# Kernel optimization log

Measured on AMD Instinct MI355X. Metric: run time of the kernel, lower is better.

The kernel has to match this reference:

```python
import jax, jax.numpy as jnp
import numpy as np

B, T, E, H = 4, 2048, 2048, 16
HD = E // H  # 128


def apply_rope(x, freqs):
    # x: (B, T, H, HD); freqs: (T, HD//2) rotation angles per position/pair
    cos = jnp.cos(freqs)[None, :, None, :]  # (1, T, 1, HD//2)
    sin = jnp.sin(freqs)[None, :, None, :]
    xr = x.reshape(*x.shape[:-1], HD // 2, 2)
    x1, x2 = xr[..., 0], xr[..., 1]
    out = jnp.stack([x1 * cos - x2 * sin, x1 * sin + x2 * cos], axis=-1)
    return out.reshape(x.shape)


def setup_inputs() -> dict:
    key = jax.random.key(0)
    k1, k2, k3, k4 = jax.random.split(key, 4)
    x = jax.random.normal(k1, (B, T, E), dtype=jnp.float32)
    freqs = jax.random.uniform(k2, (T, HD // 2), dtype=jnp.float32) * 6.28318
    w_qkv = jax.random.normal(k3, (3 * E, E), dtype=jnp.float32) * 0.02
    w_o = jax.random.normal(k4, (E, E), dtype=jnp.float32) * 0.02
    return {"x": x, "freqs": freqs, "w_qkv": w_qkv, "w_o": w_o}


def reference(x, freqs, w_qkv, w_o):
    b, t, e = x.shape
    qkv = x @ w_qkv.T                            # (B, T, 3E)
    qkv = qkv.reshape(b, t, 3, H, HD)
    q, k, v = qkv[:, :, 0], qkv[:, :, 1], qkv[:, :, 2]
    q = apply_rope(q, freqs)
    k = apply_rope(k, freqs)
    q = q.transpose(0, 2, 1, 3)                  # (B, H, T, HD)
    k = k.transpose(0, 2, 1, 3)
    v = v.transpose(0, 2, 1, 3)
    scale = 1.0 / np.sqrt(HD)
    scores = jnp.einsum('bhqd,bhkd->bhqk', q, k) * scale
    causal = jnp.tril(jnp.ones((t, t), dtype=bool))
    scores = jnp.where(causal[None, None], scores, jnp.finfo(scores.dtype).min)
    attn = jax.nn.softmax(scores, axis=-1)
    out = jnp.einsum('bhqk,bhkd->bhqd', attn, v)  # (B, H, T, HD)
    out = out.transpose(0, 2, 1, 3).reshape(b, t, e)
    return out @ w_o.T
```

## Files before the change

### kernel.cpp

```cpp
#include <hip/hip_runtime.h>
#include <type_traits>

#define DEV __device__ __forceinline__

typedef __attribute__((ext_vector_type(4))) float f32x4;
typedef __attribute__((ext_vector_type(8))) __bf16 bf16x8;
typedef __attribute__((ext_vector_type(8))) short s16x8;
typedef unsigned int u32;
typedef unsigned short u16;

DEV u16 f2bf(float f) {
  u32 u = __builtin_bit_cast(u32, f);
  u32 r = u + 0x7FFFu + ((u >> 16) & 1u);
  return (u16)(r >> 16);
}
DEV float bf2f(u16 h) {
  u32 u = ((u32)h) << 16;
  return __builtin_bit_cast(float, u);
}

template <typename A>
DEV auto mfma_sel(A a, A b, f32x4 c, int)
    -> decltype(__builtin_amdgcn_mfma_f32_16x16x32_bf16(a, b, c, 0, 0, 0)) {
  return __builtin_amdgcn_mfma_f32_16x16x32_bf16(a, b, c, 0, 0, 0);
}
template <typename A>
DEV f32x4 mfma_sel(A a, A b, f32x4 c, long) {
  using O = typename std::conditional<std::is_same<A, bf16x8>::value, s16x8, bf16x8>::type;
  return __builtin_amdgcn_mfma_f32_16x16x32_bf16(
      __builtin_bit_cast(O, a), __builtin_bit_cast(O, b), c, 0, 0, 0);
}
DEV f32x4 MFMA16(bf16x8 a, bf16x8 b, f32x4 c) { return mfma_sel(a, b, c, 0); }

DEV void gload_lds16(const void* g, void* l) {
  __builtin_amdgcn_global_load_lds(
      (__attribute__((address_space(1))) void*)(g),
      (__attribute__((address_space(3))) void*)(l), 16, 0, 0);
}

__global__ __launch_bounds__(256) void cvt_f32_bf16(const float* __restrict__ in,
                                                    u16* __restrict__ out, int n4) {
  int i = blockIdx.x * blockDim.x + threadIdx.x;
  const int stride = gridDim.x * blockDim.x;
  for (; i < n4; i += stride) {
    const float4 v = ((const float4*)in)[i];
    ushort4 o;
    o.x = f2bf(v.x); o.y = f2bf(v.y); o.z = f2bf(v.z); o.w = f2bf(v.w);
    ((ushort4*)out)[i] = o;
  }
}

__global__ __launch_bounds__(256) void build_tab(const float* __restrict__ freqs,
                                                 float* __restrict__ ct,
                                                 float* __restrict__ st, int n) {
  int i = blockIdx.x * blockDim.x + threadIdx.x;
  if (i < n) {
    float f = freqs[i];
    ct[i] = cosf(f);
    st[i] = sinf(f);
  }
}

template <bool OBF>
__global__ __launch_bounds__(512, 2) void gemm_bt(const u16* __restrict__ A,
                                                  const u16* __restrict__ Bm,
                                                  void* __restrict__ Cp,
                                                  const int M, const int N, const int K) {
  __shared__ __align__(16) u16 As[4][256 * 32];
  __shared__ __align__(16) u16 Bs[4][256 * 32];
  const int tid = threadIdx.x;
  const int wid = tid >> 6;
  const int lane = tid & 63;
  const int lrow = lane & 15;
  const int lgrp = lane >> 4;

  const int gx = gridDim.x;
  const int nwg = gx * gridDim.y;
  int id = blockIdx.y * gx + blockIdx.x;
  const int cpx = nwg >> 3;
  id = (id & 7) * cpx + (id >> 3);
  const int row0 = (id / gx) * 256;
  const int col0 = (id % gx) * 256;

  const int wm = (wid >> 2) * 128;
  const int wn = (wid & 3) * 64;

  f32x4 acc[8][4] = {};

  const int sj0 = wid * 2;
  const int srow = lane >> 2;
  const int sc = lane & 3;

#define STAGE_HALF(SLOT, T, II)                                                   \
  do {                                                                            \
    const int j_ = sj0 + (II);                                                    \
    const int row_ = j_ * 16 + srow;                                              \
    const int ch_ = sc ^ ((row_ >> 1) & 3);                                       \
    const int k0_ = (T) * 32;                                                     \
    gload_lds16(A + (size_t)(row0 + row_) * K + k0_ + ch_ * 8,                    \
                (char*)&As[SLOT][0] + j_ * 1024);                                 \
    gload_lds16(Bm + (size_t)(col0 + row_) * K + k0_ + ch_ * 8,                   \
                (char*)&Bs[SLOT][0] + j_ * 1024);                                 \
  } while (0)

#define READS_B(SLOT)                                                             \
  _Pragma("unroll") for (int fn = 0; fn < 4; ++fn) {                              \
    const int brow_ = wn + fn * 16 + lrow;                                        \
    bfr[fn] = *(const bf16x8*)((const char*)&Bs[SLOT][0] + brow_ * 64 +           \
                               ((lgrp ^ ((brow_ >> 1) & 3)) << 4));               \
  }

#define READS_A(SLOT, QUAD)                                                       \
  _Pragma("unroll") for (int i_ = 0; i_ < 4; ++i_) {                              \
    const int arow_ = wm + ((QUAD) * 4 + i_) * 16 + lrow;                         \
    af[i_] = *(const bf16x8*)((const char*)&As[SLOT][0] + arow_ * 64 +            \
                              ((lgrp ^ ((arow_ >> 1) & 3)) << 4));                \
  }

#define MFMA_QUAD(QUAD)                                                           \
  __builtin_amdgcn_s_setprio(1);                                                  \
  _Pragma("unroll") for (int fm = 0; fm < 4; ++fm) {                              \
    _Pragma("unroll") for (int fn = 0; fn < 4; ++fn)                              \
      acc[(QUAD) * 4 + fm][fn] = MFMA16(af[fm], bfr[fn], acc[(QUAD) * 4 + fm][fn]); \
  }                                                                               \
  __builtin_amdgcn_s_setprio(0);

  const int nk = K >> 5;
  STAGE_HALF(0, 0, 0); STAGE_HALF(0, 0, 1);
  STAGE_HALF(1, 1, 0); STAGE_HALF(1, 1, 1);
  STAGE_HALF(2, 2, 0); STAGE_HALF(2, 2, 1);
  __builtin_amdgcn_sched_barrier(0);
  asm volatile("s_waitcnt vmcnt(8)" ::: "memory");
  __builtin_amdgcn_s_barrier();

  bf16x8 bfr[4], af[4];
  for (int t = 0; t < nk - 2; ++t) {
    const int slot = t & 3;
    const int ns = (t + 3) & 3;
    const bool dostage = (t + 3) < nk;
    READS_B(slot)
    READS_A(slot, 0)
    if (dostage) STAGE_HALF(ns, t + 3, 0);
    __builtin_amdgcn_sched_barrier(0);
    __builtin_amdgcn_s_barrier();
    MFMA_QUAD(0)
    __builtin_amdgcn_sched_barrier(0);
    __builtin_amdgcn_s_barrier();
    READS_A(slot, 1)
    if (dostage) STAGE_HALF(ns, t + 3, 1);
    __builtin_amdgcn_sched_barrier(0);
    __builtin_amdgcn_s_barrier();
    MFMA_QUAD(1)
    __builtin_amdgcn_sched_barrier(0);
    asm volatile("s_waitcnt vmcnt(8)" ::: "memory");
    __builtin_amdgcn_s_barrier();
  }
  {
    const int slot = (nk - 2) & 3;
    READS_B(slot) READS_A(slot, 0)
    __builtin_amdgcn_sched_barrier(0);
    __builtin_amdgcn_s_barrier();
    MFMA_QUAD(0)
    __builtin_amdgcn_s_barrier();
    READS_A(slot, 1)
    __builtin_amdgcn_sched_barrier(0);
    __builtin_amdgcn_s_barrier();
    MFMA_QUAD(1)
    __builtin_amdgcn_sched_barrier(0);
    asm volatile("s_waitcnt vmcnt(0)" ::: "memory");
    __builtin_amdgcn_s_barrier();
  }
  {
    const int slot = (nk - 1) & 3;
    READS_B(slot) READS_A(slot, 0)
    __builtin_amdgcn_sched_barrier(0);
    __builtin_amdgcn_s_barrier();
    MFMA_QUAD(0)
    __builtin_amdgcn_s_barrier();
    READS_A(slot, 1)
    MFMA_QUAD(1)
  }

  #pragma unroll
  for (int fm = 0; fm < 8; ++fm) {
    #pragma unroll
    for (int r = 0; r < 4; ++r) {
      const size_t rb = (size_t)(row0 + wm + fm * 16 + lgrp * 4 + r) * N + col0 + wn + lrow;
      #pragma unroll
      for (int fn = 0; fn < 4; ++fn) {
        if constexpr (OBF)
          ((u16*)Cp)[rb + fn * 16] = f2bf(acc[fm][fn][r]);
        else
          ((float*)Cp)[rb + fn * 16] = acc[fm][fn][r];
      }
    }
  }
#undef STAGE_HALF
#undef READS_B
#undef READS_A
#undef MFMA_QUAD
}

__global__ __launch_bounds__(256) void rope_rearrange(const u16* __restrict__ qkv,
                                                      const float* __restrict__ ct,
                                                      const float* __restrict__ st,
                                                      u16* __restrict__ q_r,
                                                      u16* __restrict__ k_r,
                                                      u16* __restrict__ vt) {
  constexpr int T = 2048;
  constexpr int H = 16;
  __shared__ u16 tile[64][130];
  const int tt = blockIdx.x, h = blockIdx.y, b = blockIdx.z;
  const int t0 = tt * 64;
  const int tid = threadIdx.x;
  const int r = t0 + (tid >> 2);
  const int cg = (tid & 3) * 32;
  const int bh = b * H + h;

  #pragma unroll
  for (int which = 0; which < 2; ++which) {
    const u16* src = qkv + ((((size_t)b * T + r) * 3 + which) * H + h) * 128 + cg;
    u16* dst = (which == 0 ? q_r : k_r) + ((size_t)bh * T + r) * 128 + cg;
    const u32* su = (const u32*)src;
    u32* du = (u32*)dst;
    const int pb = r * 64 + (cg >> 1);
    #pragma unroll
    for (int p = 0; p < 16; ++p) {
      const u32 v = su[p];
      const float x1 = bf2f((u16)(v & 0xffff));
      const float x2 = bf2f((u16)(v >> 16));
      const float c = ct[pb + p];
      const float sn = st[pb + p];
      const float o1 = x1 * c - x2 * sn;
      const float o2 = x1 * sn + x2 * c;
      du[p] = (u32)f2bf(o1) | ((u32)f2bf(o2) << 16);
    }
  }

  {
    const u16* src = qkv + ((((size_t)b * T + r) * 3 + 2) * H + h) * 128 + cg;
    const int tl = tid >> 2;
    #pragma unroll
    for (int jj = 0; jj < 32; ++jj)
      tile[tl][cg + jj] = src[jj];
  }
  __syncthreads();
  {
    const int d = tid >> 1, half = tid & 1;
    u16* dst = vt + ((size_t)bh * 128 + d) * T + t0 + half * 32;
    #pragma unroll
    for (int jj = 0; jj < 32; ++jj)
      dst[jj] = tile[half * 32 + jj][d];
  }
}

__global__ __launch_bounds__(512, 2) void attn_fwd(const u16* __restrict__ Qp,
                                                   const u16* __restrict__ Kp,
                                                   const u16* __restrict__ Vp,
                                                   u16* __restrict__ Op) {
  constexpr int T = 2048;
  __shared__ __align__(16) u16 Kl[3][64 * 128];
  __shared__ __align__(16) u16 Vl[3][128 * 64];
  __shared__ __align__(16) u16 Pl[8 * 1024];

  const int tid = threadIdx.x;
  const int wid = tid >> 6;
  const int lane = tid & 63;
  const int lrow = lane & 15;
  const int lgrp = lane >> 4;

  const int lin = blockIdx.y * 4 + blockIdx.x;
  const int qa = lin >> 6;
  const int bh = ((lin & 7) << 3) | ((lin >> 3) & 7);

  const u16* Qb = Qp + (size_t)bh * T * 128;
  const u16* Kb = Kp + (size_t)bh * T * 128;
  const u16* Vb = Vp + (size_t)bh * 128 * T;

  const float CE = 0.08838834765f * 1.44269504089f;
  const float DTH = 12.0f / CE;
  const int s0 = (lane & 48) + ((lane & 48) >> 2);
  char* Pw = (char*)Pl + wid * 2048;
  const int ob = bh >> 4, oh = bh & 15;

  auto stage = [&](int buf, int kv0) {
    #pragma unroll
    for (int ii = 0; ii < 2; ++ii) {
      const int i = wid * 2 + ii;
      {
        const int rr = i * 4 + (lane >> 4);
        const int cs = (lane & 15) ^ (rr & 7);
        gload_lds16(Kb + (size_t)(kv0 + rr) * 128 + cs * 8, (char*)&Kl[buf][0] + i * 1024);
      }
      {
        const int rr = i * 8 + (lane >> 3);
        const int cs = (lane & 7) ^ (rr & 7);
        gload_lds16(Vb + (size_t)rr * T + kv0 + cs * 8, (char*)&Vl[buf][0] + i * 1024);
      }
    }
  };

  auto process = [&](const int qi) {
    const int q0 = qi * 256;
    const int wq0 = q0 + wid * 32;

    bf16x8 qf[2][4];
    #pragma unroll
    for (int qg = 0; qg < 2; ++qg) {
      const int qrow = wq0 + qg * 16 + lrow;
      #pragma unroll
      for (int db = 0; db < 4; ++db)
        qf[qg][db] = *(const bf16x8*)(Qb + (size_t)qrow * 128 + db * 32 + lgrp * 8);
    }

    f32x4 o[2][8] = {};
    float m[2] = {-3e38f, -3e38f};
    float l[2] = {0.f, 0.f};

    const int nkv = 4 * qi + 4;
    stage(0, 0);
    stage(1, 64);
    int cs = 0;
    for (int j = 0; j < nkv; ++j) {
      __builtin_amdgcn_sched_barrier(0);
      if (j < nkv - 1) {
        asm volatile("s_waitcnt vmcnt(4)" ::: "memory");
      } else {
        asm volatile("s_waitcnt vmcnt(0)" ::: "memory");
      }
      __builtin_amdgcn_s_barrier();
      if (j + 2 < nkv) {
        int ss = cs + 2; if (ss >= 3) ss -= 3;
        stage(ss, (j + 2) * 64);
      }
      const int kv0 = j * 64;

      if (kv0 <= wq0 + 31) {
        f32x4 s[2][4] = {};
        #pragma unroll
        for (int t4 = 0; t4 < 4; ++t4) {
          const int krow = t4 * 16 + lrow;
          #pragma unroll
          for (int db = 0; db < 4; ++db) {
            const int ch = (db * 4 + lgrp) ^ (krow & 7);
            bf16x8 kf = *(const bf16x8*)((const char*)&Kl[cs][0] + krow * 256 + ch * 16);
            s[0][t4] = MFMA16(kf, qf[0][db], s[0][t4]);
            s[1][t4] = MFMA16(kf, qf[1][db], s[1][t4]);
          }
        }

        if (kv0 + 63 > wq0) {
          #pragma unroll
          for (int qg = 0; qg < 2; ++qg) {
            const int lim = wq0 + qg * 16 + lrow - kv0 - lgrp * 4;
            #pragma unroll
            for (int t4 = 0; t4 < 4; ++t4) {
              #pragma unroll
              for (int r = 0; r < 4; ++r)
                if (t4 * 16 + r > lim) s[qg][t4][r] = -3e38f;
            }
          }
        }

        float pmax[2];
        #pragma unroll
        for (int qg = 0; qg < 2; ++qg) {
          float pm = fmaxf(fmaxf(s[qg][0][0], s[qg][0][1]), fmaxf(s[qg][0][2], s[qg][0][3]));
          #pragma unroll
          for (int t4 = 1; t4 < 4; ++t4)
            pm = fmaxf(pm, fmaxf(fmaxf(s[qg][t4][0], s[qg][t4][1]),
                                 fmaxf(s[qg][t4][2], s[qg][t4][3])));
          pm = fmaxf(pm, __shfl_xor(pm, 16));
          pm = fmaxf(pm, __shfl_xor(pm, 32));
          pmax[qg] = pm;
        }

        float alpha[2] = {1.f, 1.f};
        const float dmax = fmaxf(pmax[0] - m[0], pmax[1] - m[1]);
        if (__any(dmax > DTH)) {
          #pragma unroll
          for (int qg = 0; qg < 2; ++qg) {
            const float mn = fmaxf(m[qg], pmax[qg]);
            alpha[qg] = exp2f((m[qg] - mn) * CE);
            m[qg] = mn;
          }
          #pragma unroll
          for (int qg = 0; qg < 2; ++qg) {
            #pragma unroll
            for (int r = 0; r < 4; ++r) {
              const float a4 = __shfl(alpha[qg], s0 + r);
              #pragma unroll
              for (int db = 0; db < 8; ++db)
                o[qg][db][r] *= a4;
            }
          }
        }

        #pragma unroll
        for (int qg = 0; qg < 2; ++qg) {
          float psum = 0.f;
          #pragma unroll
          for (int t4 = 0; t4 < 4; ++t4) {
            #pragma unroll
            for (int r = 0; r < 4; ++r) {
              const float p = exp2f((s[qg][t4][r] - m[qg]) * CE);
              s[qg][t4][r] = p;
              psum += p;
            }
          }
          psum += __shfl_xor(psum, 16);
          psum += __shfl_xor(psum, 32);
          l[qg] = l[qg] * alpha[qg] + psum;

          #pragma unroll
          for (int t4 = 0; t4 < 4; ++t4) {
            uint2 w;
            w.x = (u32)f2bf(s[qg][t4][0]) | ((u32)f2bf(s[qg][t4][1]) << 16);
            w.y = (u32)f2bf(s[qg][t4][2]) | ((u32)f2bf(s[qg][t4][3]) << 16);
            const int off = lrow * 128 + (((t4 * 2 + (lgrp >> 1)) ^ (lrow & 7)) << 4) + (lgrp & 1) * 8;
            *(uint2*)(Pw + off) = w;
          }
          asm volatile("s_waitcnt lgkmcnt(0)" ::: "memory");
          __builtin_amdgcn_sched_barrier(0);

          bf16x8 pa[2];
          #pragma unroll
          for (int kb = 0; kb < 2; ++kb)
            pa[kb] = *(const bf16x8*)(Pw + lrow * 128 + (((kb * 4 + lgrp) ^ (lrow & 7)) << 4));
          #pragma unroll
          for (int db = 0; db < 8; ++db) {
            const int vrow = db * 16 + lrow;
            #pragma unroll
            for (int kb = 0; kb < 2; ++kb) {
              const int vch = (kb * 4 + lgrp) ^ (vrow & 7);
              bf16x8 vf = *(const bf16x8*)((const char*)&Vl[cs][0] + vrow * 128 + vch * 16);
              o[qg][db] = MFMA16(pa[kb], vf, o[qg][db]);
            }
          }
        }
      }
      cs = (cs == 2) ? 0 : cs + 1;
    }

    #pragma unroll
    for (int qg = 0; qg < 2; ++qg) {
      const float inv = 1.f / l[qg];
      float inv4[4];
      #pragma unroll
      for (int r = 0; r < 4; ++r) inv4[r] = __shfl(inv, s0 + r);
      #pragma unroll
      for (int db = 0; db < 8; ++db) {
        #pragma unroll
        for (int r = 0; r < 4; ++r) {
          const int qrow = wq0 + qg * 16 + lgrp * 4 + r;
          Op[((size_t)ob * T + qrow) * 2048 + oh * 128 + db * 16 + lrow] =
              f2bf(o[qg][db][r] * inv4[r]);
        }
      }
    }
  };

  process(7 - qa);
  __syncthreads();
  process(qa);
}

extern "C" void kernel_launch(void* const* d_in, const int* in_sizes, int n_in,
                              void* d_out, int out_size, void* d_ws, size_t ws_size,
                              hipStream_t stream) {
  const float* x = (const float*)d_in[0];
  const float* freqs = (const float*)d_in[1];
  const float* w_qkv = (const float*)d_in[2];
  const float* w_o = (const float*)d_in[3];

  constexpr int B = 4, T = 2048, E = 2048, H = 16;
  constexpr size_t M = (size_t)B * T;
  constexpr int N3 = 3 * E;

  char* ws = (char*)d_ws;
  size_t off = 0;
  auto alloc = [&](size_t bytes) {
    void* p = ws + off;
    off += (bytes + 255) & ~(size_t)255;
    return p;
  };
  u16* wqkv_bf = (u16*)alloc((size_t)N3 * E * 2);
  u16* wo_bf   = (u16*)alloc((size_t)E * E * 2);
  u16* x_bf    = (u16*)alloc(M * E * 2);
  u16* qkv_bf  = (u16*)alloc(M * (size_t)N3 * 2);
  u16* k_r     = (u16*)alloc(M * E * 2);
  u16* vt      = (u16*)alloc(M * E * 2);
  float* ct    = (float*)alloc((size_t)T * 64 * 4);
  float* st    = (float*)alloc((size_t)T * 64 * 4);
  u16* q_r = x_bf;
  u16* attn_o = qkv_bf;

  cvt_f32_bf16<<<2048, 256, 0, stream>>>(x, x_bf, (int)(M * E / 4));
  cvt_f32_bf16<<<2048, 256, 0, stream>>>(w_qkv, wqkv_bf, N3 * E / 4);
  cvt_f32_bf16<<<2048, 256, 0, stream>>>(w_o, wo_bf, E * E / 4);
  build_tab<<<(T * 64) / 256, 256, 0, stream>>>(freqs, ct, st, T * 64);

  gemm_bt<true><<<dim3(N3 / 256, (int)(M / 256)), 512, 0, stream>>>(
      x_bf, wqkv_bf, qkv_bf, (int)M, N3, E);
  rope_rearrange<<<dim3(T / 64, H, B), 256, 0, stream>>>(qkv_bf, ct, st, q_r, k_r, vt);
  attn_fwd<<<dim3(4, B * H), 512, 0, stream>>>(q_r, k_r, vt, attn_o);
  gemm_bt<false><<<dim3(E / 256, (int)(M / 256)), 512, 0, stream>>>(
      attn_o, wo_bf, d_out, (int)M, E, E);
}
```

Before: 483.4 us.

## Deepen attention K/V prefetch to four stages and unify GEMM main loop

The attention kernel's K/V shared-memory ring grows from 3 to 4 slots, so three tiles are prefetched ahead instead of two. The vmcnt wait thresholds are adjusted for the deeper queue, and slot indexing becomes a simple j&3. The GEMM loop folds its two peeled tail iterations into the main loop, with vmcnt waits chosen per iteration. It also places the workgroup barrier before an explicit lgkmcnt(0) wait ahead of each MFMA quad. The deeper ring raises LDS use to about 144KB per block, which could limit residency. The barrier reordering changes how LDS reads overlap with the MFMAs.

```diff
diff --git a/kernel.cpp b/kernel.cpp
--- a/kernel.cpp
+++ b/kernel.cpp
@@ -129,56 +129,34 @@
   STAGE_HALF(0, 0, 0); STAGE_HALF(0, 0, 1);
   STAGE_HALF(1, 1, 0); STAGE_HALF(1, 1, 1);
   STAGE_HALF(2, 2, 0); STAGE_HALF(2, 2, 1);
-  __builtin_amdgcn_sched_barrier(0);
   asm volatile("s_waitcnt vmcnt(8)" ::: "memory");
   __builtin_amdgcn_s_barrier();
 
   bf16x8 bfr[4], af[4];
-  for (int t = 0; t < nk - 2; ++t) {
+  for (int t = 0; t < nk; ++t) {
     const int slot = t & 3;
     const int ns = (t + 3) & 3;
     const bool dostage = (t + 3) < nk;
     READS_B(slot)
     READS_A(slot, 0)
     if (dostage) STAGE_HALF(ns, t + 3, 0);
+    __builtin_amdgcn_s_barrier();
+    asm volatile("s_waitcnt lgkmcnt(0)" ::: "memory");
     __builtin_amdgcn_sched_barrier(0);
-    __builtin_amdgcn_s_barrier();
     MFMA_QUAD(0)
-    __builtin_amdgcn_sched_barrier(0);
     __builtin_amdgcn_s_barrier();
     READS_A(slot, 1)
     if (dostage) STAGE_HALF(ns, t + 3, 1);
+    __builtin_amdgcn_s_barrier();
+    asm volatile("s_waitcnt lgkmcnt(0)" ::: "memory");
     __builtin_amdgcn_sched_barrier(0);
-    __builtin_amdgcn_s_barrier();
     MFMA_QUAD(1)
-    __builtin_amdgcn_sched_barrier(0);
-    asm volatile("s_waitcnt vmcnt(8)" ::: "memory");
-    __builtin_amdgcn_s_barrier();
-  }
-  {
-    const int slot = (nk - 2) & 3;
-    READS_B(slot) READS_A(slot, 0)
-    __builtin_amdgcn_sched_barrier(0);
-    __builtin_amdgcn_s_barrier();
-    MFMA_QUAD(0)
-    __builtin_amdgcn_s_barrier();
-    READS_A(slot, 1)
-    __builtin_amdgcn_sched_barrier(0);
-    __builtin_amdgcn_s_barrier();
-    MFMA_QUAD(1)
-    __builtin_amdgcn_sched_barrier(0);
-    asm volatile("s_waitcnt vmcnt(0)" ::: "memory");
-    __builtin_amdgcn_s_barrier();
-  }
-  {
-    const int slot = (nk - 1) & 3;
-    READS_B(slot) READS_A(slot, 0)
-    __builtin_amdgcn_sched_barrier(0);
-    __builtin_amdgcn_s_barrier();
-    MFMA_QUAD(0)
-    __builtin_amdgcn_s_barrier();
-    READS_A(slot, 1)
-    MFMA_QUAD(1)
+    if (t < nk - 1) {
+      if (t <= nk - 4)      asm volatile("s_waitcnt vmcnt(8)" ::: "memory");
+      else if (t == nk - 3) asm volatile("s_waitcnt vmcnt(4)" ::: "memory");
+      else                  asm volatile("s_waitcnt vmcnt(0)" ::: "memory");
+      __builtin_amdgcn_s_barrier();
+    }
   }
 
   #pragma unroll
@@ -259,8 +237,8 @@
                                                    const u16* __restrict__ Vp,
                                                    u16* __restrict__ Op) {
   constexpr int T = 2048;
-  __shared__ __align__(16) u16 Kl[3][64 * 128];
-  __shared__ __align__(16) u16 Vl[3][128 * 64];
+  __shared__ __align__(16) u16 Kl[4][64 * 128];
+  __shared__ __align__(16) u16 Vl[4][128 * 64];
   __shared__ __align__(16) u16 Pl[8 * 1024];
 
   const int tid = threadIdx.x;
@@ -320,19 +298,14 @@
     const int nkv = 4 * qi + 4;
     stage(0, 0);
     stage(1, 64);
-    int cs = 0;
+    stage(2, 128);
     for (int j = 0; j < nkv; ++j) {
-      __builtin_amdgcn_sched_barrier(0);
-      if (j < nkv - 1) {
-        asm volatile("s_waitcnt vmcnt(4)" ::: "memory");
-      } else {
-        asm volatile("s_waitcnt vmcnt(0)" ::: "memory");
-      }
+      if (j <= nkv - 3)      asm volatile("s_waitcnt vmcnt(8)" ::: "memory");
+      else if (j == nkv - 2) asm volatile("s_waitcnt vmcnt(4)" ::: "memory");
+      else                   asm volatile("s_waitcnt vmcnt(0)" ::: "memory");
       __builtin_amdgcn_s_barrier();
-      if (j + 2 < nkv) {
-        int ss = cs + 2; if (ss >= 3) ss -= 3;
-        stage(ss, (j + 2) * 64);
-      }
+      if (j + 3 < nkv) stage((j + 3) & 3, (j + 3) * 64);
+      const int cs = j & 3;
       const int kv0 = j * 64;
 
       if (kv0 <= wq0 + 31) {
@@ -439,7 +412,6 @@
           }
         }
       }
-      cs = (cs == 2) ? 0 : cs + 1;
     }
 
     #pragma unroll
```

New measurement: 491.3 us. No clear change (+1.6%).

## Fuse RoPE and head rearrangement into QKV GEMM epilogue; deepen attention KV pipeline

Applied to the files above, without the earlier changes.

The QKV GEMM epilogue now applies RoPE, using a lane shuffle to fetch the paired element and a packed cos/sin table, and writes Q, K and V directly in per-head layout. This removes the separate rope_rearrange pass that re-read the full qkv buffer. V is still transposed by a smaller separate kernel. The attention kernel also grows its K/V staging ring from 3 to 4 buffers with a prefetch distance of 3, at the cost of more LDS, which may lower occupancy.

```diff
diff --git a/kernel.cpp b/kernel.cpp
--- a/kernel.cpp
+++ b/kernel.cpp
@@ -50,21 +50,23 @@
   }
 }
 
-__global__ __launch_bounds__(256) void build_tab(const float* __restrict__ freqs,
-                                                 float* __restrict__ ct,
-                                                 float* __restrict__ st, int n) {
+__global__ __launch_bounds__(256) void build_cst(const float* __restrict__ freqs,
+                                                 float2* __restrict__ cst, int n) {
   int i = blockIdx.x * blockDim.x + threadIdx.x;
   if (i < n) {
     float f = freqs[i];
-    ct[i] = cosf(f);
-    st[i] = sinf(f);
-  }
-}
-
-template <bool OBF>
+    cst[i] = make_float2(cosf(f), sinf(f));
+  }
+}
+
+template <int MODE>
 __global__ __launch_bounds__(512, 2) void gemm_bt(const u16* __restrict__ A,
                                                   const u16* __restrict__ Bm,
                                                   void* __restrict__ Cp,
+                                                  u16* __restrict__ q_r,
+                                                  u16* __restrict__ k_r,
+                                                  u16* __restrict__ v_r,
+                                                  const float2* __restrict__ cst,
                                                   const int M, const int N, const int K) {
   __shared__ __align__(16) u16 As[4][256 * 32];
   __shared__ __align__(16) u16 Bs[4][256 * 32];
@@ -181,17 +183,46 @@
     MFMA_QUAD(1)
   }
 
-  #pragma unroll
-  for (int fm = 0; fm < 8; ++fm) {
-    #pragma unroll
-    for (int r = 0; r < 4; ++r) {
-      const size_t rb = (size_t)(row0 + wm + fm * 16 + lgrp * 4 + r) * N + col0 + wn + lrow;
+  if constexpr (MODE == 0) {
+    #pragma unroll
+    for (int fm = 0; fm < 8; ++fm) {
       #pragma unroll
-      for (int fn = 0; fn < 4; ++fn) {
-        if constexpr (OBF)
-          ((u16*)Cp)[rb + fn * 16] = f2bf(acc[fm][fn][r]);
-        else
+      for (int r = 0; r < 4; ++r) {
+        const size_t rb = (size_t)(row0 + wm + fm * 16 + lgrp * 4 + r) * N + col0 + wn + lrow;
+        #pragma unroll
+        for (int fn = 0; fn < 4; ++fn)
           ((float*)Cp)[rb + fn * 16] = acc[fm][fn][r];
+      }
+    }
+  } else {
+    const int which = col0 >> 11;
+    const int colw = (col0 & 2047) + wn;
+    const int h = colw >> 7;
+    const int d0 = colw & 127;
+    u16* const dst0 = (which == 0) ? q_r : (which == 1) ? k_r : v_r;
+    const bool isv = (which == 2);
+    #pragma unroll
+    for (int fm = 0; fm < 8; ++fm) {
+      #pragma unroll
+      for (int r = 0; r < 4; ++r) {
+        const int grow = row0 + wm + fm * 16 + lgrp * 4 + r;
+        const int bb = grow >> 11, tt = grow & 2047;
+        u16* const drow = dst0 + (((size_t)(bb * 16 + h) * 2048 + tt) << 7);
+        if (isv) {
+          #pragma unroll
+          for (int fn = 0; fn < 4; ++fn)
+            drow[d0 + fn * 16 + lrow] = f2bf(acc[fm][fn][r]);
+        } else {
+          #pragma unroll
+          for (int fn = 0; fn < 4; ++fn) {
+            const float v = acc[fm][fn][r];
+            const float p = __shfl_xor(v, 1);
+            const int d = d0 + fn * 16 + lrow;
+            const float2 cs = cst[tt * 64 + (d >> 1)];
+            const float o = (lrow & 1) ? (p * cs.y + v * cs.x) : (v * cs.x - p * cs.y);
+            drow[d] = f2bf(o);
+          }
+        }
       }
     }
   }
@@ -201,45 +232,17 @@
 #undef MFMA_QUAD
 }
 
-__global__ __launch_bounds__(256) void rope_rearrange(const u16* __restrict__ qkv,
-                                                      const float* __restrict__ ct,
-                                                      const float* __restrict__ st,
-                                                      u16* __restrict__ q_r,
-                                                      u16* __restrict__ k_r,
-                                                      u16* __restrict__ vt) {
+__global__ __launch_bounds__(256) void vtrans(const u16* __restrict__ vr,
+                                              u16* __restrict__ vt) {
   constexpr int T = 2048;
-  constexpr int H = 16;
   __shared__ u16 tile[64][130];
-  const int tt = blockIdx.x, h = blockIdx.y, b = blockIdx.z;
-  const int t0 = tt * 64;
+  const int t0 = blockIdx.x * 64;
+  const int bh = blockIdx.y;
   const int tid = threadIdx.x;
-  const int r = t0 + (tid >> 2);
-  const int cg = (tid & 3) * 32;
-  const int bh = b * H + h;
-
-  #pragma unroll
-  for (int which = 0; which < 2; ++which) {
-    const u16* src = qkv + ((((size_t)b * T + r) * 3 + which) * H + h) * 128 + cg;
-    u16* dst = (which == 0 ? q_r : k_r) + ((size_t)bh * T + r) * 128 + cg;
-    const u32* su = (const u32*)src;
-    u32* du = (u32*)dst;
-    const int pb = r * 64 + (cg >> 1);
-    #pragma unroll
-    for (int p = 0; p < 16; ++p) {
-      const u32 v = su[p];
-      const float x1 = bf2f((u16)(v & 0xffff));
-      const float x2 = bf2f((u16)(v >> 16));
-      const float c = ct[pb + p];
-      const float sn = st[pb + p];
-      const float o1 = x1 * c - x2 * sn;
-      const float o2 = x1 * sn + x2 * c;
-      du[p] = (u32)f2bf(o1) | ((u32)f2bf(o2) << 16);
-    }
-  }
-
   {
-    const u16* src = qkv + ((((size_t)b * T + r) * 3 + 2) * H + h) * 128 + cg;
     const int tl = tid >> 2;
+    const int cg = (tid & 3) * 32;
+    const u16* src = vr + ((size_t)bh * T + t0 + tl) * 128 + cg;
     #pragma unroll
     for (int jj = 0; jj < 32; ++jj)
       tile[tl][cg + jj] = src[jj];
@@ -259,8 +262,8 @@
                                                    const u16* __restrict__ Vp,
                                                    u16* __restrict__ Op) {
   constexpr int T = 2048;
-  __shared__ __align__(16) u16 Kl[3][64 * 128];
-  __shared__ __align__(16) u16 Vl[3][128 * 64];
+  __shared__ __align__(16) u16 Kl[4][64 * 128];
+  __shared__ __align__(16) u16 Vl[4][128 * 64];
   __shared__ __align__(16) u16 Pl[8 * 1024];
 
   const int tid = threadIdx.x;
@@ -320,19 +323,14 @@
     const int nkv = 4 * qi + 4;
     stage(0, 0);
     stage(1, 64);
-    int cs = 0;
+    stage(2, 128);
     for (int j = 0; j < nkv; ++j) {
-      __builtin_amdgcn_sched_barrier(0);
-      if (j < nkv - 1) {
-        asm volatile("s_waitcnt vmcnt(4)" ::: "memory");
-      } else {
-        asm volatile("s_waitcnt vmcnt(0)" ::: "memory");
-      }
+      if (j <= nkv - 3)      asm volatile("s_waitcnt vmcnt(8)" ::: "memory");
+      else if (j == nkv - 2) asm volatile("s_waitcnt vmcnt(4)" ::: "memory");
+      else                   asm volatile("s_waitcnt vmcnt(0)" ::: "memory");
       __builtin_amdgcn_s_barrier();
-      if (j + 2 < nkv) {
-        int ss = cs + 2; if (ss >= 3) ss -= 3;
-        stage(ss, (j + 2) * 64);
-      }
+      if (j + 3 < nkv) stage((j + 3) & 3, (j + 3) * 64);
+      const int cs = j & 3;
       const int kv0 = j * 64;
 
       if (kv0 <= wq0 + 31) {
@@ -439,7 +437,6 @@
           }
         }
       }
-      cs = (cs == 2) ? 0 : cs + 1;
     }
 
     #pragma unroll
@@ -487,23 +484,22 @@
   u16* wqkv_bf = (u16*)alloc((size_t)N3 * E * 2);
   u16* wo_bf   = (u16*)alloc((size_t)E * E * 2);
   u16* x_bf    = (u16*)alloc(M * E * 2);
-  u16* qkv_bf  = (u16*)alloc(M * (size_t)N3 * 2);
+  u16* q_r     = (u16*)alloc(M * E * 2);
   u16* k_r     = (u16*)alloc(M * E * 2);
+  u16* v_r     = (u16*)alloc(M * E * 2);
   u16* vt      = (u16*)alloc(M * E * 2);
-  float* ct    = (float*)alloc((size_t)T * 64 * 4);
-  float* st    = (float*)alloc((size_t)T * 64 * 4);
-  u16* q_r = x_bf;
-  u16* attn_o = qkv_bf;
+  u16* attn_o  = (u16*)alloc(M * E * 2);
+  float2* cst  = (float2*)alloc((size_t)T * 64 * 8);
 
   cvt_f32_bf16<<<2048, 256, 0, stream>>>(x, x_bf, (int)(M * E / 4));
   cvt_f32_bf16<<<2048, 256, 0, stream>>>(w_qkv, wqkv_bf, N3 * E / 4);
   cvt_f32_bf16<<<2048, 256, 0, stream>>>(w_o, wo_bf, E * E / 4);
-  build_tab<<<(T * 64) / 256, 256, 0, stream>>>(freqs, ct, st, T * 64);
-
-  gemm_bt<true><<<dim3(N3 / 256, (int)(M / 256)), 512, 0, stream>>>(
-      x_bf, wqkv_bf, qkv_bf, (int)M, N3, E);
-  rope_rearrange<<<dim3(T / 64, H, B), 256, 0, stream>>>(qkv_bf, ct, st, q_r, k_r, vt);
+  build_cst<<<(T * 64) / 256, 256, 0, stream>>>(freqs, cst, T * 64);
+
+  gemm_bt<2><<<dim3(N3 / 256, (int)(M / 256)), 512, 0, stream>>>(
+      x_bf, wqkv_bf, nullptr, q_r, k_r, v_r, cst, (int)M, N3, E);
+  vtrans<<<dim3(T / 64, B * H), 256, 0, stream>>>(v_r, vt);
   attn_fwd<<<dim3(4, B * H), 512, 0, stream>>>(q_r, k_r, vt, attn_o);
-  gemm_bt<false><<<dim3(E / 256, (int)(M / 256)), 512, 0, stream>>>(
-      attn_o, wo_bf, d_out, (int)M, E, E);
-}
+  gemm_bt<0><<<dim3(E / 256, (int)(M / 256)), 512, 0, stream>>>(
+      attn_o, wo_bf, d_out, nullptr, nullptr, nullptr, nullptr, (int)M, E, E);
+}
```

New measurement: 465.8 us. 1.04x faster.
